# Performance work log

Hardware: AMD Instinct MI355X
Metric: run time of the kernel (lower is better)

Reference implementation:

```python
import jax, jax.numpy as jnp
import numpy as np


def _apply_1q(state, gate, wire):
    # state: (N,2,2,2,2) complex; gate: (2,2) shared or (N,2,2) per-circuit
    s = jnp.moveaxis(state, wire + 1, 1)
    shp = s.shape
    s = s.reshape(shp[0], 2, -1)
    if gate.ndim == 3:
        s = jnp.einsum('nab,nbr->nar', gate, s)
    else:
        s = jnp.einsum('ab,nbr->nar', gate, s)
    return jnp.moveaxis(s.reshape(shp), 1, wire + 1)


def _apply_cnot(state, c, t):
    # flip target axis where control axis == 1 (c < t assumed)
    s = jnp.moveaxis(state, (c + 1, t + 1), (1, 2))
    s = jnp.stack([s[:, 0], s[:, 1, ::-1]], axis=1)
    return jnp.moveaxis(s, (1, 2), (c + 1, t + 1))


def _simulate(angles, params):
    # angles: (N,4) float32 RY encoding angles; params: (layers,4,3) Rot params
    N = angles.shape[0]
    state = jnp.zeros((N, 2, 2, 2, 2), jnp.complex64).at[:, 0, 0, 0, 0].set(1.0)
    half = angles * 0.5
    ca, sa = jnp.cos(half), jnp.sin(half)
    for w in range(4):
        c, s = ca[:, w], sa[:, w]
        gate = jnp.stack([jnp.stack([c, -s], -1), jnp.stack([s, c], -1)], -2).astype(jnp.complex64)
        state = _apply_1q(state, gate, w)
    for layer in range(params.shape[0]):
        for w in range(4):
            phi, theta, omega = params[layer, w, 0], params[layer, w, 1], params[layer, w, 2]
            ct, st = jnp.cos(theta * 0.5), jnp.sin(theta * 0.5)
            # PennyLane Rot(phi,theta,omega) = RZ(omega) RY(theta) RZ(phi)
            g00 = jnp.exp(-1j * (phi + omega) * 0.5) * ct
            g01 = -jnp.exp(1j * (phi - omega) * 0.5) * st
            g10 = jnp.exp(-1j * (phi - omega) * 0.5) * st
            g11 = jnp.exp(1j * (phi + omega) * 0.5) * ct
            gate = jnp.stack([jnp.stack([g00, g01]), jnp.stack([g10, g11])]).astype(jnp.complex64)
            state = _apply_1q(state, gate, w)
        state = _apply_cnot(state, 0, 1)  # range(0, 3, 2): (0,1),(2,3)
        state = _apply_cnot(state, 2, 3)
        state = _apply_cnot(state, 1, 2)  # range(1, 3, 2): (1,2)
    probs = jnp.abs(state) ** 2  # (N,2,2,2,2) float32
    z = []
    for w in range(4):
        p = jnp.moveaxis(probs, w + 1, 1)
        z.append(jnp.sum(p[:, 0], axis=(1, 2, 3)) - jnp.sum(p[:, 1], axis=(1, 2, 3)))
    return jnp.stack(z, axis=-1)  # (N,4) <Z_w> expectations


def setup_inputs() -> dict:
    key = jax.random.key(0)
    k1, k2, k3 = jax.random.split(key, 3)
    B = 1024
    x = jax.random.normal(k1, (B, 1, 28, 28), jnp.float32)
    params = jax.random.normal(k2, (2, 4, 3), jnp.float32)
    head_w = jax.random.normal(k3, (10, 4 * 14 * 14), jnp.float32) * 0.02
    head_b = jnp.zeros((10,), jnp.float32)
    return {"x": x, "params": params, "head_w": head_w, "head_b": head_b}


def reference(x, params, head_w, head_b):
    B = x.shape[0]
    img = x.reshape(B, 28, 28)
    # 2x2 patches, stride 2; patch order row-major over (r,c), row-major within patch
    patches = img.reshape(B, 14, 2, 14, 2).transpose(0, 1, 3, 2, 4).reshape(B * 196, 4)
    feats = _simulate(patches, params).reshape(B, 196 * 4)  # matches torch.cat(patches, dim=1)
    logits = feats @ head_w.T + head_b
    return jax.nn.log_softmax(logits, axis=-1)
```

## Files before the change

kernel.cpp:

```cpp
#include <hip/hip_runtime.h>
#include <math.h>

__global__ __launch_bounds__(256) void quanv_fused_kernel(
    const float* __restrict__ x,
    const float* __restrict__ params,
    const float* __restrict__ head_w,
    const float* __restrict__ head_b,
    float* __restrict__ out,
    int B)
{
    __shared__ float col[4][8];
    __shared__ float Mw[4][4];
    __shared__ float feats[784];
    __shared__ float red[10][4];
    __shared__ float logits_s[10];

    const int tid = threadIdx.x;
    const int b   = blockIdx.x;

    if (tid < 4) {
        const float phi   = params[tid * 3 + 0];
        const float theta = params[tid * 3 + 1];
        const float omega = params[tid * 3 + 2];
        const float cph = __cosf(phi),   sph = __sinf(phi);
        const float cth = __cosf(theta), sth = __sinf(theta);
        const float com = __cosf(omega), som = __sinf(omega);
        col[tid][0] = cth * cph * com - sph * som;
        col[tid][1] = cth * cph * som + sph * com;
        col[tid][2] = -sth * cph;
        col[tid][4] = sth * com;
        col[tid][5] = sth * som;
        col[tid][6] = cth;
    } else if (tid < 8) {
        const int w = tid - 4;
        const float phi   = params[12 + w * 3 + 0];
        const float theta = params[12 + w * 3 + 1];
        const float sth = __sinf(theta);
        Mw[w][0] = __cosf(theta);
        Mw[w][1] = -sth * __cosf(phi);
        Mw[w][2] = -sth * __sinf(phi);
    }
    __syncthreads();

    if (tid < 196) {
        const int pi_ = tid / 14, pj = tid % 14;
        const float* img = x + (size_t)b * 784;
        const float2 row0 = *(const float2*)(img + (2 * pi_)     * 28 + 2 * pj);
        const float2 row1 = *(const float2*)(img + (2 * pi_ + 1) * 28 + 2 * pj);
        const float a[4] = { row0.x, row0.y, row1.x, row1.y };

        float u0[4], u1[4], qre[4], qim[4], zb[4];
#pragma unroll
        for (int w = 0; w < 4; w++) {
            const float sa = __sinf(a[w]), ca = __cosf(a[w]);
            const float xx = fmaf(sa, col[w][0], ca * col[w][4]);
            const float yy = fmaf(sa, col[w][1], ca * col[w][5]);
            const float zz = fmaf(sa, col[w][2], ca * col[w][6]);
            zb[w]  = zz;
            u0[w]  = 0.5f + 0.5f * zz;
            u1[w]  = 0.5f - 0.5f * zz;
            qre[w] = 0.5f * xx;
            qim[w] = 0.5f * yy;
        }
        const float e0 = u0[0], e1 = u1[0], ze = zb[0], qr = qre[0], qi = qim[0];
        const float f0 = u0[1], f1 = u1[1], zf = zb[1], rr = qre[1], ri = qim[1];
        const float g0 = u0[2], g1 = u1[2], zg = zb[2], sr = qre[2], si = qim[2];
        const float h0 = u0[3], h1 = u1[3], zh = zb[3], tr = qre[3], ti = qim[3];

        const float m0 = Mw[0][0], w0r = Mw[0][1], w0i = Mw[0][2];
        const float m1 = Mw[1][0], w1r = Mw[1][1], w1i = Mw[1][2];
        const float m2 = Mw[2][0], w2r = Mw[2][1], w2i = Mw[2][2];
        const float m3 = Mw[3][0], w3r = Mw[3][1], w3i = Mw[3][2];

        const float pb   = 4.0f * tr * sr;
        const float PBi  = 2.0f * tr * si;
        const float w2s_m = w2r * sr - w2i * si;
        const float w2s_p = w2r * sr + w2i * si;
        const float Ga  = fmaf(m2, zg,  4.0f * tr * w2s_m);
        const float Gb  = fmaf(-m2, zg, 4.0f * tr * w2s_p);
        const float Gcr = w2r;
        const float Gci = fmaf(w2i, zg, 2.0f * m2 * PBi);

        const float w3t_m = w3r * tr - w3i * ti;
        const float w3t_p = w3r * tr + w3i * ti;
        const float alpha = fmaf(m3, zh, 2.0f * w3t_m);
        const float beta  = fmaf(-m3, zh, 2.0f * w3t_p);
        const float dq    = g0 * alpha - g1 * beta;
        const float Kr = w3r;
        const float Ki = fmaf(2.0f * m3, ti, w3i * zh);
        const float Tr = sr * Kr - si * Ki;
        const float Ti = sr * Ki + si * Kr;
        const float ZA = ze * zf;
        const float z3 = fmaf(ZA, fmaf(m2, dq, -2.0f * w2i * Ti), 2.0f * w2r * Tr);

        const float z0 = fmaf(m0, ze, 4.0f * rr * (w0r * qr - w0i * qi));

        const float w1r_m = w1r * rr - w1i * ri;
        const float w1r_p = w1r * rr + w1i * ri;
        const float gam1  = fmaf(m1, zf, 2.0f * pb * w1r_m);
        const float del1  = fmaf(-m1, zf, 2.0f * pb * w1r_p);
        const float diag1 = e0 * gam1 - e1 * del1;
        const float L1r = pb * w1r;
        const float L1i = fmaf(2.0f * m1, ri, pb * w1i * zf);
        const float QL1r = qr * L1r - qi * L1i;
        const float QL1i = qr * L1i + qi * L1r;
        const float z1 = fmaf(m0, diag1, 2.0f * (w0r * QL1r - w0i * QL1i));

        const float Wgr = w1r * Gcr - w1i * Gci;
        const float Wgi = w1r * Gci + w1i * Gcr;
        const float gam2 = fmaf(m1, Ga * f0 - Gb * f1, 2.0f * (Wgr * rr - Wgi * ri));
        const float del2 = fmaf(m1, Ga * f1 - Gb * f0, 2.0f * (Wgr * rr + Wgi * ri));
        const float diag2 = e0 * gam2 - e1 * del2;
        const float L2r = fmaf(m1 * (Ga - Gb), rr, Wgr);
        const float L2i = fmaf(m1 * (Ga + Gb), ri, Wgi * zf);
        const float QL2r = qr * L2r - qi * L2i;
        const float QL2i = qr * L2i + qi * L2r;
        const float z2 = fmaf(m0, diag2, 2.0f * (w0r * QL2r - w0i * QL2i));

        feats[tid * 4 + 0] = z0;
        feats[tid * 4 + 1] = z1;
        feats[tid * 4 + 2] = z2;
        feats[tid * 4 + 3] = z3;
    }
    __syncthreads();

    float acc[10];
#pragma unroll
    for (int k = 0; k < 10; k++) acc[k] = 0.0f;
#pragma unroll
    for (int i = 0; i < 3; i++) {
        const int j = tid + i * 256;
        const float f = feats[j];
#pragma unroll
        for (int k = 0; k < 10; k++) acc[k] = fmaf(f, head_w[k * 784 + j], acc[k]);
    }
    if (tid < 16) {
        const int j = tid + 768;
        const float f = feats[j];
#pragma unroll
        for (int k = 0; k < 10; k++) acc[k] = fmaf(f, head_w[k * 784 + j], acc[k]);
    }
    const int lane = tid & 63, wid = tid >> 6;
#pragma unroll
    for (int k = 0; k < 10; k++) {
        float v = acc[k];
#pragma unroll
        for (int off = 32; off > 0; off >>= 1) v += __shfl_down(v, off, 64);
        if (lane == 0) red[k][wid] = v;
    }
    __syncthreads();
    if (tid < 10) {
        logits_s[tid] = red[tid][0] + red[tid][1] + red[tid][2] + red[tid][3]
                        + head_b[tid];
    }
    __syncthreads();
    if (tid == 0) {
        float mx = logits_s[0];
#pragma unroll
        for (int k = 1; k < 10; k++) mx = fmaxf(mx, logits_s[k]);
        float sum = 0.0f;
#pragma unroll
        for (int k = 0; k < 10; k++) sum += __expf(logits_s[k] - mx);
        const float lse = __logf(sum);
        float* o = out + (size_t)b * 10;
#pragma unroll
        for (int k = 0; k < 10; k++) o[k] = logits_s[k] - mx - lse;
    }
}

extern "C" void kernel_launch(void* const* d_in, const int* in_sizes, int n_in,
                              void* d_out, int out_size, void* d_ws, size_t ws_size,
                              hipStream_t stream) {
    const float* x      = (const float*)d_in[0];
    const float* params = (const float*)d_in[1];
    const float* head_w = (const float*)d_in[2];
    const float* head_b = (const float*)d_in[3];
    float* out = (float*)d_out;

    const int B = in_sizes[0] / 784;

    quanv_fused_kernel<<<B, 256, 0, stream>>>(x, params, head_w, head_b, out, B);
}
```

Measured before the change: 11.32 us.

## Process two images per block and restructure head GEMV reduction

Each block now handles two images, with 392 patch threads spread over two passes, so the block count is halved and the params setup and head_w reads are shared across two images. The head matvec is remapped so 8-lane groups each own one (image, class) pair and reduce with width-8 shuffles, which removes the cross-wave shared-memory reduction and one barrier. Softmax is parallelised over 20 threads instead of a single thread. The trade-off is fewer, longer blocks and an uneven pass split, plus strided shared-memory reads of feats in the GEMV.

```diff
diff --git a/kernel.cpp b/kernel.cpp
--- a/kernel.cpp
+++ b/kernel.cpp
@@ -11,12 +11,12 @@
 {
     __shared__ float col[4][8];
     __shared__ float Mw[4][4];
-    __shared__ float feats[784];
-    __shared__ float red[10][4];
-    __shared__ float logits_s[10];
+    __shared__ float feats[2][784];
+    __shared__ float logits_s[2][10];
 
     const int tid = threadIdx.x;
     const int b   = blockIdx.x;
+    const int nimg = (2 * b + 2 <= B) ? 2 : (B - 2 * b);
 
     if (tid < 4) {
         const float phi   = params[tid * 3 + 0];
@@ -42,129 +42,126 @@
     }
     __syncthreads();
 
-    if (tid < 196) {
-        const int pi_ = tid / 14, pj = tid % 14;
-        const float* img = x + (size_t)b * 784;
-        const float2 row0 = *(const float2*)(img + (2 * pi_)     * 28 + 2 * pj);
-        const float2 row1 = *(const float2*)(img + (2 * pi_ + 1) * 28 + 2 * pj);
-        const float a[4] = { row0.x, row0.y, row1.x, row1.y };
+#pragma unroll
+    for (int pass = 0; pass < 2; ++pass) {
+        const int p = tid + (pass << 8);
+        if (p < nimg * 196) {
+            const int im = (p >= 196) ? 1 : 0;
+            const int lp = p - im * 196;
+            const int pi_ = lp / 14, pj = lp % 14;
+            const float* img = x + (size_t)(2 * b + im) * 784;
+            const float2 row0 = *(const float2*)(img + (2 * pi_)     * 28 + 2 * pj);
+            const float2 row1 = *(const float2*)(img + (2 * pi_ + 1) * 28 + 2 * pj);
+            const float a[4] = { row0.x, row0.y, row1.x, row1.y };
 
-        float u0[4], u1[4], qre[4], qim[4], zb[4];
+            float u0[4], u1[4], qre[4], qim[4], zb[4];
 #pragma unroll
-        for (int w = 0; w < 4; w++) {
-            const float sa = __sinf(a[w]), ca = __cosf(a[w]);
-            const float xx = fmaf(sa, col[w][0], ca * col[w][4]);
-            const float yy = fmaf(sa, col[w][1], ca * col[w][5]);
-            const float zz = fmaf(sa, col[w][2], ca * col[w][6]);
-            zb[w]  = zz;
-            u0[w]  = 0.5f + 0.5f * zz;
-            u1[w]  = 0.5f - 0.5f * zz;
-            qre[w] = 0.5f * xx;
-            qim[w] = 0.5f * yy;
+            for (int w = 0; w < 4; w++) {
+                const float sa = __sinf(a[w]), ca = __cosf(a[w]);
+                const float xx = fmaf(sa, col[w][0], ca * col[w][4]);
+                const float yy = fmaf(sa, col[w][1], ca * col[w][5]);
+                const float zz = fmaf(sa, col[w][2], ca * col[w][6]);
+                zb[w]  = zz;
+                u0[w]  = 0.5f + 0.5f * zz;
+                u1[w]  = 0.5f - 0.5f * zz;
+                qre[w] = 0.5f * xx;
+                qim[w] = 0.5f * yy;
+            }
+            const float e0 = u0[0], e1 = u1[0], ze = zb[0], qr = qre[0], qi = qim[0];
+            const float f0 = u0[1], f1 = u1[1], zf = zb[1], rr = qre[1], ri = qim[1];
+            const float g0 = u0[2], g1 = u1[2], zg = zb[2], sr = qre[2], si = qim[2];
+            const float zh = zb[3], tr = qre[3], ti = qim[3];
+
+            const float m0 = Mw[0][0], w0r = Mw[0][1], w0i = Mw[0][2];
+            const float m1 = Mw[1][0], w1r = Mw[1][1], w1i = Mw[1][2];
+            const float m2 = Mw[2][0], w2r = Mw[2][1], w2i = Mw[2][2];
+            const float m3 = Mw[3][0], w3r = Mw[3][1], w3i = Mw[3][2];
+
+            const float pb   = 4.0f * tr * sr;
+            const float PBi  = 2.0f * tr * si;
+            const float w2s_m = w2r * sr - w2i * si;
+            const float w2s_p = w2r * sr + w2i * si;
+            const float Ga  = fmaf(m2, zg,  4.0f * tr * w2s_m);
+            const float Gb  = fmaf(-m2, zg, 4.0f * tr * w2s_p);
+            const float Gcr = w2r;
+            const float Gci = fmaf(w2i, zg, 2.0f * m2 * PBi);
+
+            const float w3t_m = w3r * tr - w3i * ti;
+            const float w3t_p = w3r * tr + w3i * ti;
+            const float alpha = fmaf(m3, zh, 2.0f * w3t_m);
+            const float beta  = fmaf(-m3, zh, 2.0f * w3t_p);
+            const float dq    = g0 * alpha - g1 * beta;
+            const float Kr = w3r;
+            const float Ki = fmaf(2.0f * m3, ti, w3i * zh);
+            const float Tr = sr * Kr - si * Ki;
+            const float Ti = sr * Ki + si * Kr;
+            const float ZA = ze * zf;
+            const float z3 = fmaf(ZA, fmaf(m2, dq, -2.0f * w2i * Ti), 2.0f * w2r * Tr);
+
+            const float z0 = fmaf(m0, ze, 4.0f * rr * (w0r * qr - w0i * qi));
+
+            const float w1r_m = w1r * rr - w1i * ri;
+            const float w1r_p = w1r * rr + w1i * ri;
+            const float gam1  = fmaf(m1, zf, 2.0f * pb * w1r_m);
+            const float del1  = fmaf(-m1, zf, 2.0f * pb * w1r_p);
+            const float diag1 = e0 * gam1 - e1 * del1;
+            const float L1r = pb * w1r;
+            const float L1i = fmaf(2.0f * m1, ri, pb * w1i * zf);
+            const float QL1r = qr * L1r - qi * L1i;
+            const float QL1i = qr * L1i + qi * L1r;
+            const float z1 = fmaf(m0, diag1, 2.0f * (w0r * QL1r - w0i * QL1i));
+
+            const float Wgr = w1r * Gcr - w1i * Gci;
+            const float Wgi = w1r * Gci + w1i * Gcr;
+            const float gam2 = fmaf(m1, Ga * f0 - Gb * f1, 2.0f * (Wgr * rr - Wgi * ri));
+            const float del2 = fmaf(m1, Ga * f1 - Gb * f0, 2.0f * (Wgr * rr + Wgi * ri));
+            const float diag2 = e0 * gam2 - e1 * del2;
+            const float L2r = fmaf(m1 * (Ga - Gb), rr, Wgr);
+            const float L2i = fmaf(m1 * (Ga + Gb), ri, Wgi * zf);
+            const float QL2r = qr * L2r - qi * L2i;
+            const float QL2i = qr * L2i + qi * L2r;
+            const float z2 = fmaf(m0, diag2, 2.0f * (w0r * QL2r - w0i * QL2i));
+
+            *(float4*)&feats[im][lp * 4] = make_float4(z0, z1, z2, z3);
         }
-        const float e0 = u0[0], e1 = u1[0], ze = zb[0], qr = qre[0], qi = qim[0];
-        const float f0 = u0[1], f1 = u1[1], zf = zb[1], rr = qre[1], ri = qim[1];
-        const float g0 = u0[2], g1 = u1[2], zg = zb[2], sr = qre[2], si = qim[2];
-        const float h0 = u0[3], h1 = u1[3], zh = zb[3], tr = qre[3], ti = qim[3];
-
-        const float m0 = Mw[0][0], w0r = Mw[0][1], w0i = Mw[0][2];
-        const float m1 = Mw[1][0], w1r = Mw[1][1], w1i = Mw[1][2];
-        const float m2 = Mw[2][0], w2r = Mw[2][1], w2i = Mw[2][2];
-        const float m3 = Mw[3][0], w3r = Mw[3][1], w3i = Mw[3][2];
-
-        const float pb   = 4.0f * tr * sr;
-        const float PBi  = 2.0f * tr * si;
-        const float w2s_m = w2r * sr - w2i * si;
-        const float w2s_p = w2r * sr + w2i * si;
-        const float Ga  = fmaf(m2, zg,  4.0f * tr * w2s_m);
-        const float Gb  = fmaf(-m2, zg, 4.0f * tr * w2s_p);
-        const float Gcr = w2r;
-        const float Gci = fmaf(w2i, zg, 2.0f * m2 * PBi);
-
-        const float w3t_m = w3r * tr - w3i * ti;
-        const float w3t_p = w3r * tr + w3i * ti;
-        const float alpha = fmaf(m3, zh, 2.0f * w3t_m);
-        const float beta  = fmaf(-m3, zh, 2.0f * w3t_p);
-        const float dq    = g0 * alpha - g1 * beta;
-        const float Kr = w3r;
-        const float Ki = fmaf(2.0f * m3, ti, w3i * zh);
-        const float Tr = sr * Kr - si * Ki;
-        const float Ti = sr * Ki + si * Kr;
-        const float ZA = ze * zf;
-        const float z3 = fmaf(ZA, fmaf(m2, dq, -2.0f * w2i * Ti), 2.0f * w2r * Tr);
-
-        const float z0 = fmaf(m0, ze, 4.0f * rr * (w0r * qr - w0i * qi));
-
-        const float w1r_m = w1r * rr - w1i * ri;
-        const float w1r_p = w1r * rr + w1i * ri;
-        const float gam1  = fmaf(m1, zf, 2.0f * pb * w1r_m);
-        const float del1  = fmaf(-m1, zf, 2.0f * pb * w1r_p);
-        const float diag1 = e0 * gam1 - e1 * del1;
-        const float L1r = pb * w1r;
-        const float L1i = fmaf(2.0f * m1, ri, pb * w1i * zf);
-        const float QL1r = qr * L1r - qi * L1i;
-        const float QL1i = qr * L1i + qi * L1r;
-        const float z1 = fmaf(m0, diag1, 2.0f * (w0r * QL1r - w0i * QL1i));
-
-        const float Wgr = w1r * Gcr - w1i * Gci;
-        const float Wgi = w1r * Gci + w1i * Gcr;
-        const float gam2 = fmaf(m1, Ga * f0 - Gb * f1, 2.0f * (Wgr * rr - Wgi * ri));
-        const float del2 = fmaf(m1, Ga * f1 - Gb * f0, 2.0f * (Wgr * rr + Wgi * ri));
-        const float diag2 = e0 * gam2 - e1 * del2;
-        const float L2r = fmaf(m1 * (Ga - Gb), rr, Wgr);
-        const float L2i = fmaf(m1 * (Ga + Gb), ri, Wgi * zf);
-        const float QL2r = qr * L2r - qi * L2i;
-        const float QL2i = qr * L2i + qi * L2r;
-        const float z2 = fmaf(m0, diag2, 2.0f * (w0r * QL2r - w0i * QL2i));
-
-        feats[tid * 4 + 0] = z0;
-        feats[tid * 4 + 1] = z1;
-        feats[tid * 4 + 2] = z2;
-        feats[tid * 4 + 3] = z3;
     }
     __syncthreads();
 
-    float acc[10];
+    if (tid < 160) {
+        const int im = tid / 80;
+        const int r  = tid - im * 80;
+        const int k  = r >> 3, g = r & 7;
+        if (im < nimg) {
+            const float* hw = head_w + k * 784;
+            const float* fv = feats[im];
+            float acc0 = 0.0f, acc1 = 0.0f;
 #pragma unroll
-    for (int k = 0; k < 10; k++) acc[k] = 0.0f;
-#pragma unroll
-    for (int i = 0; i < 3; i++) {
-        const int j = tid + i * 256;
-        const float f = feats[j];
-#pragma unroll
-        for (int k = 0; k < 10; k++) acc[k] = fmaf(f, head_w[k * 784 + j], acc[k]);
-    }
-    if (tid < 16) {
-        const int j = tid + 768;
-        const float f = feats[j];
-#pragma unroll
-        for (int k = 0; k < 10; k++) acc[k] = fmaf(f, head_w[k * 784 + j], acc[k]);
-    }
-    const int lane = tid & 63, wid = tid >> 6;
-#pragma unroll
-    for (int k = 0; k < 10; k++) {
-        float v = acc[k];
-#pragma unroll
-        for (int off = 32; off > 0; off >>= 1) v += __shfl_down(v, off, 64);
-        if (lane == 0) red[k][wid] = v;
+            for (int i = 0; i < 98; i += 2) {
+                const int j0 = g + (i << 3);
+                acc0 = fmaf(fv[j0],     hw[j0],     acc0);
+                acc1 = fmaf(fv[j0 + 8], hw[j0 + 8], acc1);
+            }
+            float v = acc0 + acc1;
+            v += __shfl_down(v, 4, 8);
+            v += __shfl_down(v, 2, 8);
+            v += __shfl_down(v, 1, 8);
+            if (g == 0) logits_s[im][k] = v + head_b[k];
+        }
     }
     __syncthreads();
-    if (tid < 10) {
-        logits_s[tid] = red[tid][0] + red[tid][1] + red[tid][2] + red[tid][3]
-                        + head_b[tid];
-    }
-    __syncthreads();
-    if (tid == 0) {
-        float mx = logits_s[0];
+
+    if (tid < 20) {
+        const int im = tid / 10, k = tid - im * 10;
+        if (im < nimg) {
+            const float* l = logits_s[im];
+            float mx = l[0];
 #pragma unroll
-        for (int k = 1; k < 10; k++) mx = fmaxf(mx, logits_s[k]);
-        float sum = 0.0f;
+            for (int j = 1; j < 10; j++) mx = fmaxf(mx, l[j]);
+            float sum = 0.0f;
 #pragma unroll
-        for (int k = 0; k < 10; k++) sum += __expf(logits_s[k] - mx);
-        const float lse = __logf(sum);
-        float* o = out + (size_t)b * 10;
-#pragma unroll
-        for (int k = 0; k < 10; k++) o[k] = logits_s[k] - mx - lse;
+            for (int j = 0; j < 10; j++) sum += __expf(l[j] - mx);
+            out[(size_t)(2 * b + im) * 10 + k] = l[k] - mx - __logf(sum);
+        }
     }
 }
 
@@ -178,6 +175,7 @@
     float* out = (float*)d_out;
 
     const int B = in_sizes[0] / 784;
+    const int nblocks = (B + 1) / 2;
 
-    quanv_fused_kernel<<<B, 256, 0, stream>>>(x, params, head_w, head_b, out, B);
+    quanv_fused_kernel<<<nblocks, 256, 0, stream>>>(x, params, head_w, head_b, out, B);
 }
```

Measured after the change: 12.57 us. 11.1% more time.
